# Optimization experiments

Hardware: AMD Instinct MI355X
Metric: run time of the kernel (lower is better)

Reference implementation:

```python
import jax, jax.numpy as jnp
import numpy as np

BS, GRID, LSTM_H, CNN_C, PROJ = 256, 49, 512, 2048, 512


def setup_inputs() -> dict:
    key = jax.random.key(0)
    ks = jax.random.split(key, 7)
    s = lambda fan_in: 1.0 / np.sqrt(fan_in)
    return {
        "lstm_hidden": jax.random.normal(ks[0], (BS, LSTM_H), jnp.float32),
        "cnn_feat": jax.random.normal(ks[1], (BS, GRID, CNN_C), jnp.float32),
        "W_lstm": jax.random.normal(ks[2], (PROJ, LSTM_H), jnp.float32) * s(LSTM_H),
        "b_lstm": jax.random.normal(ks[3], (PROJ,), jnp.float32) * s(LSTM_H),
        "W_cnn": jax.random.normal(ks[4], (PROJ, CNN_C), jnp.float32) * s(CNN_C),
        "b_cnn": jax.random.normal(ks[5], (PROJ,), jnp.float32) * s(CNN_C),
        "w_attn": jax.random.normal(ks[6], (1, PROJ), jnp.float32) * s(PROJ),
    }


def reference(lstm_hidden, cnn_feat, W_lstm, b_lstm, W_cnn, b_cnn, w_attn):
    # H computed once (original loop recomputes it per grid, identically)
    H = lstm_hidden @ W_lstm.T + b_lstm                       # (bs, P)
    V = jnp.einsum("bgc,pc->bgp", cnn_feat, W_cnn) + b_cnn    # (bs, G, P)
    z = jnp.tanh(H[:, None, :] + V) @ w_attn[0]               # (bs, G)
    bs, G = z.shape
    # Faithful to torch: cat over grids along dim 0 -> (G*bs,), then view(bs, G)
    z_scrambled = jnp.swapaxes(z, 0, 1).reshape(bs, G)
    return jax.nn.softmax(z_scrambled, axis=1)
```

## Files before the change

kernel.cpp:

```cpp
#include <hip/hip_runtime.h>
#include <math.h>

#define BSZ    256
#define GRID_N 49
#define LSTMH  512
#define CNN_C  2048
#define PROJ   512
#define KAUG   2560
#define M_TOT  12544
#define BK     64
#define KTILES (KAUG / BK)

#define MT     64
#define NT     128
#define NBLK   ((M_TOT / MT) * (PROJ / NT))

#define ACHUNKS (M_TOT * CNN_C / 8)
#define LCHUNKS (BSZ * LSTMH / 8)
#define ABLK    ((ACHUNKS + LCHUNKS) / 256)
#define WBLK    640
#define PBLK    (ABLK + WBLK)

typedef short bf16x8 __attribute__((ext_vector_type(8)));
typedef float f32x4  __attribute__((ext_vector_type(4)));

static __device__ __forceinline__ unsigned short bf16_rne(float f) {
    unsigned int u = __float_as_uint(f);
    u = u + 0x7FFFu + ((u >> 16) & 1u);
    return (unsigned short)(u >> 16);
}
static __device__ __forceinline__ uint4 pack8f(const float* f) {
    uint4 o;
    o.x = (unsigned int)bf16_rne(f[0]) | ((unsigned int)bf16_rne(f[1]) << 16);
    o.y = (unsigned int)bf16_rne(f[2]) | ((unsigned int)bf16_rne(f[3]) << 16);
    o.z = (unsigned int)bf16_rne(f[4]) | ((unsigned int)bf16_rne(f[5]) << 16);
    o.w = (unsigned int)bf16_rne(f[6]) | ((unsigned int)bf16_rne(f[7]) << 16);
    return o;
}
static __device__ __forceinline__ float tanh_fast(float x) {
    float e = __expf(2.f * x);
    return 1.f - 2.f / (e + 1.f);
}
static __device__ __forceinline__ void glds16(const void* g, void* l) {
    __builtin_amdgcn_global_load_lds(
        (const __attribute__((address_space(1))) unsigned int*)g,
        (__attribute__((address_space(3))) unsigned int*)l, 16, 0, 0);
}

__global__ __launch_bounds__(256) void prep_all(
    const float* __restrict__ cnn, const float* __restrict__ lstm,
    const float* __restrict__ Wc,  const float* __restrict__ Wl,
    unsigned short* __restrict__ wsW, unsigned short* __restrict__ wsA,
    unsigned short* __restrict__ wsL, float* __restrict__ out)
{
    const int bid = blockIdx.x, t = threadIdx.x;
    if (bid < 49) out[bid * 256 + t] = 0.f;
    float f[8];
    if (bid < ABLK) {
        const int c = bid * 256 + t;
        const float* src; unsigned short* dst;
        if (c < ACHUNKS) { src = cnn  + (size_t)c * 8; dst = wsA + (size_t)c * 8; }
        else { const int c2 = c - ACHUNKS; src = lstm + (size_t)c2 * 8; dst = wsL + (size_t)c2 * 8; }
        *(float4*)&f[0] = ((const float4*)src)[0];
        *(float4*)&f[4] = ((const float4*)src)[1];
        *(uint4*)dst = pack8f(f);
    } else {
        const int c  = (bid - ABLK) * 256 + t;
        const int p  = c / 320;
        const int kc = (c % 320) * 8;
        const float* src = (kc < CNN_C) ? (Wc + (size_t)p * CNN_C + kc)
                                        : (Wl + (size_t)p * LSTMH + (kc - CNN_C));
        *(float4*)&f[0] = ((const float4*)src)[0];
        *(float4*)&f[4] = ((const float4*)src)[1];
        *(uint4*)(wsW + (size_t)p * KAUG + kc) = pack8f(f);
    }
}

__global__ __launch_bounds__(256, 4) void gemm6(
    const unsigned short* __restrict__ wsW, const unsigned short* __restrict__ wsA,
    const unsigned short* __restrict__ wsL,
    const float* __restrict__ bl, const float* __restrict__ bc,
    const float* __restrict__ wat, float* __restrict__ out)
{
    __shared__ unsigned short Ash[MT][BK];
    __shared__ unsigned short Bsh[NT][BK];

    const int t   = threadIdx.x;
    const int w   = t >> 6;
    const int l   = t & 63;
    const int q   = l >> 4;
    const int r16 = l & 15;

    const int bid = (int)blockIdx.x;
    const int swz = (bid & 7) * (NBLK / 8) + (bid >> 3);
    const int m0  = (swz >> 2) * MT;
    const int n0  = (swz & 3) * NT;

    const int srow = l >> 3;
    const int cg   = (l & 7) ^ srow;

    auto stage = [&](int kt) {
        const int k0 = kt * BK;
        #pragma unroll
        for (int j = 0; j < 4; ++j) {
            const int rowb = w * 32 + j * 8;
            const unsigned short* g = wsW + (size_t)(n0 + rowb + srow) * KAUG + k0 + cg * 8;
            glds16(g, &Bsh[rowb][0]);
        }
        if (k0 < CNN_C) {
            #pragma unroll
            for (int j = 0; j < 2; ++j) {
                const int rowa = w * 16 + j * 8;
                const unsigned short* g = wsA + (size_t)(m0 + rowa + srow) * CNN_C + k0 + cg * 8;
                glds16(g, &Ash[rowa][0]);
            }
        } else {
            const int k0l = k0 - CNN_C;
            #pragma unroll
            for (int j = 0; j < 2; ++j) {
                const int rowa = w * 16 + j * 8;
                const int rg   = m0 + rowa + srow;
                const unsigned short* g = wsL + (size_t)(rg / 49) * LSTMH + k0l + cg * 8;
                glds16(g, &Ash[rowa][0]);
            }
        }
    };

    f32x4 acc[4][2];
    #pragma unroll
    for (int mt = 0; mt < 4; ++mt)
        #pragma unroll
        for (int nt = 0; nt < 2; ++nt)
            acc[mt][nt] = (f32x4){0.f, 0.f, 0.f, 0.f};

    stage(0);

    for (int kt = 0; kt < KTILES; ++kt) {
        asm volatile("s_waitcnt vmcnt(0)" ::: "memory");
        __builtin_amdgcn_s_barrier();
        #pragma unroll
        for (int ks = 0; ks < 2; ++ks) {
            const int cp = ((ks * 4 + q) ^ (r16 & 7)) * 8;
            bf16x8 af[4], bfr[2];
            #pragma unroll
            for (int mt = 0; mt < 4; ++mt)
                af[mt] = *(const bf16x8*)&Ash[mt * 16 + r16][cp];
            #pragma unroll
            for (int nt = 0; nt < 2; ++nt)
                bfr[nt] = *(const bf16x8*)&Bsh[w * 32 + nt * 16 + r16][cp];
            #pragma unroll
            for (int mt = 0; mt < 4; ++mt)
                #pragma unroll
                for (int nt = 0; nt < 2; ++nt)
                    acc[mt][nt] = __builtin_amdgcn_mfma_f32_16x16x32_bf16(
                        af[mt], bfr[nt], acc[mt][nt], 0, 0, 0);
        }
        __builtin_amdgcn_s_barrier();
        if (kt + 1 < KTILES) stage(kt + 1);
    }

    float* zpf = (float*)&Ash[0][0];
    float part[4][4];
    #pragma unroll
    for (int mt = 0; mt < 4; ++mt)
        #pragma unroll
        for (int rr = 0; rr < 4; ++rr) part[mt][rr] = 0.f;
    #pragma unroll
    for (int nt = 0; nt < 2; ++nt) {
        const int p = n0 + w * 32 + nt * 16 + r16;
        const float bb = bl[p] + bc[p];
        const float wa = wat[p];
        #pragma unroll
        for (int mt = 0; mt < 4; ++mt)
            #pragma unroll
            for (int rr = 0; rr < 4; ++rr)
                part[mt][rr] += tanh_fast(acc[mt][nt][rr] + bb) * wa;
    }
    #pragma unroll
    for (int mt = 0; mt < 4; ++mt)
        #pragma unroll
        for (int rr = 0; rr < 4; ++rr) {
            float v = part[mt][rr];
            v += __shfl_xor(v, 1);
            v += __shfl_xor(v, 2);
            v += __shfl_xor(v, 4);
            v += __shfl_xor(v, 8);
            if (r16 == 0) zpf[w * MT + mt * 16 + q * 4 + rr] = v;
        }
    __syncthreads();
    if (t < MT) {
        const float v = zpf[t] + zpf[MT + t] + zpf[2 * MT + t] + zpf[3 * MT + t];
        const int row = m0 + t;
        const int b2  = row / 49;
        const int g2  = row - b2 * 49;
        atomicAdd(&out[g2 * BSZ + b2], v);
    }
}

__global__ __launch_bounds__(256, 4) void gemm_k(
    const float* __restrict__ lstm, const float* __restrict__ cnn,
    const float* __restrict__ Wc,   const float* __restrict__ Wl,
    const float* __restrict__ bl,   const float* __restrict__ bc,
    const float* __restrict__ wat,  float* __restrict__ out)
{
    __shared__ unsigned short Ash[MT][BK];
    __shared__ unsigned short Bsh[NT][BK];
    __shared__ float zp[4][MT];

    const int t   = threadIdx.x;
    const int w   = t >> 6;
    const int l   = t & 63;
    const int q   = l >> 4;
    const int r16 = l & 15;

    const int bid = (int)blockIdx.x;
    const int swz = (bid & 7) * (NBLK / 8) + (bid >> 3);
    const int m0 = (swz >> 2) * MT;
    const int n0 = (swz & 3) * NT;

    const int ra  = t >> 2;
    const int ca0 = t & 3;
    const int sa  = ra & 7;
    const int grow = m0 + ra;
    const int ab   = grow / 49;
    const int ag   = grow - ab * 49;
    const float* cnnb  = cnn + ((size_t)ab * GRID_N + ag) * CNN_C;
    const float* lstmb = lstm + (size_t)ab * LSTMH;

    f32x4 acc[4][2];
    #pragma unroll
    for (int mt = 0; mt < 4; ++mt)
        #pragma unroll
        for (int nt = 0; nt < 2; ++nt)
            acc[mt][nt] = (f32x4){0.f, 0.f, 0.f, 0.f};

    float4 fa0, fa1, fa2, fa3;

    auto a_load = [&](int k0) {
        const float* s = (k0 < CNN_C) ? (cnnb + k0) : (lstmb + (k0 - CNN_C));
        const float4* p0 = (const float4*)(s + ca0 * 8);
        const float4* p1 = (const float4*)(s + (ca0 + 4) * 8);
        fa0 = p0[0]; fa1 = p0[1];
        fa2 = p1[0]; fa3 = p1[1];
    };
    auto a_write = [&]() {
        float f[8];
        *(float4*)&f[0] = fa0; *(float4*)&f[4] = fa1;
        *(uint4*)&Ash[ra][(ca0 ^ sa) * 8] = pack8f(f);
        *(float4*)&f[0] = fa2; *(float4*)&f[4] = fa3;
        *(uint4*)&Ash[ra][((ca0 + 4) ^ sa) * 8] = pack8f(f);
    };
    auto b_stage = [&](int k0) {
        const int rb = t >> 1;
        const int hb = t & 1;
        const float* s = (k0 < CNN_C) ? (Wc + (size_t)(n0 + rb) * CNN_C + k0)
                                      : (Wl + (size_t)(n0 + rb) * LSTMH + (k0 - CNN_C));
        const int sw = rb & 7;
        #pragma unroll
        for (int c = 0; c < 4; ++c) {
            const int cc = hb * 4 + c;
            float f[8];
            *(float4*)&f[0] = ((const float4*)(s + cc * 8))[0];
            *(float4*)&f[4] = ((const float4*)(s + cc * 8))[1];
            *(uint4*)&Bsh[rb][(cc ^ sw) * 8] = pack8f(f);
        }
    };

    a_load(0);
    a_write();
    b_stage(0);

    for (int kt = 0; kt < KTILES; ++kt) {
        __syncthreads();
        const bool more = (kt + 1 < KTILES);
        if (more) a_load((kt + 1) * BK);
        #pragma unroll
        for (int ks = 0; ks < 2; ++ks) {
            const int cp = ((ks * 4 + q) ^ (r16 & 7)) * 8;
            bf16x8 af[4], bfr[2];
            #pragma unroll
            for (int mt = 0; mt < 4; ++mt)
                af[mt] = *(const bf16x8*)&Ash[mt * 16 + r16][cp];
            #pragma unroll
            for (int nt = 0; nt < 2; ++nt)
                bfr[nt] = *(const bf16x8*)&Bsh[w * 32 + nt * 16 + r16][cp];
            #pragma unroll
            for (int mt = 0; mt < 4; ++mt)
                #pragma unroll
                for (int nt = 0; nt < 2; ++nt)
                    acc[mt][nt] = __builtin_amdgcn_mfma_f32_16x16x32_bf16(
                        af[mt], bfr[nt], acc[mt][nt], 0, 0, 0);
        }
        __syncthreads();
        if (more) { a_write(); b_stage((kt + 1) * BK); }
    }

    float part[4][4];
    #pragma unroll
    for (int mt = 0; mt < 4; ++mt)
        #pragma unroll
        for (int rr = 0; rr < 4; ++rr) part[mt][rr] = 0.f;
    #pragma unroll
    for (int nt = 0; nt < 2; ++nt) {
        const int p = n0 + w * 32 + nt * 16 + r16;
        const float bb = bl[p] + bc[p];
        const float wa = wat[p];
        #pragma unroll
        for (int mt = 0; mt < 4; ++mt)
            #pragma unroll
            for (int rr = 0; rr < 4; ++rr)
                part[mt][rr] += tanh_fast(acc[mt][nt][rr] + bb) * wa;
    }
    #pragma unroll
    for (int mt = 0; mt < 4; ++mt)
        #pragma unroll
        for (int rr = 0; rr < 4; ++rr) {
            float v = part[mt][rr];
            v += __shfl_xor(v, 1);
            v += __shfl_xor(v, 2);
            v += __shfl_xor(v, 4);
            v += __shfl_xor(v, 8);
            if (r16 == 0) zp[w][mt * 16 + q * 4 + rr] = v;
        }
    __syncthreads();
    if (t < MT) {
        const float v = zp[0][t] + zp[1][t] + zp[2][t] + zp[3][t];
        const int row = m0 + t;
        const int b2  = row / 49;
        const int g2  = row - b2 * 49;
        atomicAdd(&out[g2 * BSZ + b2], v);
    }
}

__global__ __launch_bounds__(64) void softmax_rows(float* __restrict__ out)
{
    const int i = blockIdx.x;
    const int j = threadIdx.x;
    float x = (j < GRID_N) ? out[i * GRID_N + j] : -1e30f;
    float m = x;
    #pragma unroll
    for (int off = 32; off > 0; off >>= 1) m = fmaxf(m, __shfl_xor(m, off));
    float e = (j < GRID_N) ? __expf(x - m) : 0.f;
    float s = e;
    #pragma unroll
    for (int off = 32; off > 0; off >>= 1) s += __shfl_xor(s, off);
    if (j < GRID_N) out[i * GRID_N + j] = e / s;
}

extern "C" void kernel_launch(void* const* d_in, const int* in_sizes, int n_in,
                              void* d_out, int out_size, void* d_ws, size_t ws_size,
                              hipStream_t stream)
{
    const float* lstm = (const float*)d_in[0];
    const float* cnn  = (const float*)d_in[1];
    const float* Wl   = (const float*)d_in[2];
    const float* bl   = (const float*)d_in[3];
    const float* Wc   = (const float*)d_in[4];
    const float* bc   = (const float*)d_in[5];
    const float* wat  = (const float*)d_in[6];
    float* out = (float*)d_out;

    const size_t szW = (size_t)PROJ * KAUG * sizeof(unsigned short);
    const size_t szA = (size_t)M_TOT * CNN_C * sizeof(unsigned short);
    const size_t szL = (size_t)BSZ * LSTMH * sizeof(unsigned short);

    if (ws_size >= szW + szA + szL) {
        unsigned short* wsW = (unsigned short*)d_ws;
        unsigned short* wsA = wsW + (size_t)PROJ * KAUG;
        unsigned short* wsL = wsA + (size_t)M_TOT * CNN_C;
        prep_all<<<dim3(PBLK), dim3(256), 0, stream>>>(cnn, lstm, Wc, Wl, wsW, wsA, wsL, out);
        gemm6<<<dim3(NBLK), dim3(256), 0, stream>>>(wsW, wsA, wsL, bl, bc, wat, out);
    } else {
        hipMemsetAsync(out, 0, (size_t)out_size * sizeof(float), stream);
        gemm_k<<<dim3(NBLK), dim3(256), 0, stream>>>(lstm, cnn, Wc, Wl, bl, bc, wat, out);
    }
    softmax_rows<<<dim3(BSZ), dim3(64), 0, stream>>>(out);
}
```

Baseline: 219.1 us.

## Double-buffer GEMM LDS tiles and use grid-stride loop in prep kernel

The GEMM now keeps two LDS buffers for A and B and issues the global-to-LDS loads for the next K tile before computing on the current one, so memory latency overlaps with MFMA work and only one barrier is needed per iteration. The prep kernel switches from one chunk per thread to a grid-stride loop over a fixed 1792-block grid that covers activations, LSTM and weights together. Double buffering doubles LDS use per block (to 48KB), which may cut occupancy below the four blocks per CU requested by the launch bounds.

Result: slower. 245.6 us (+12.1%).

```diff
diff --git a/kernel.cpp b/kernel.cpp
--- a/kernel.cpp
+++ b/kernel.cpp
@@ -17,9 +17,10 @@
 
 #define ACHUNKS (M_TOT * CNN_C / 8)
 #define LCHUNKS (BSZ * LSTMH / 8)
-#define ABLK    ((ACHUNKS + LCHUNKS) / 256)
-#define WBLK    640
-#define PBLK    (ABLK + WBLK)
+#define WCHUNKS (PROJ * KAUG / 8)
+#define TOTCHUNK (ACHUNKS + LCHUNKS + WCHUNKS)
+#define PGRID   1792
+#define PSTEP   (PGRID * 256)
 
 typedef short bf16x8 __attribute__((ext_vector_type(8)));
 typedef float f32x4  __attribute__((ext_vector_type(4)));
@@ -47,7 +48,7 @@
         (__attribute__((address_space(3))) unsigned int*)l, 16, 0, 0);
 }
 
-__global__ __launch_bounds__(256) void prep_all(
+__global__ __launch_bounds__(256) void prep_all2(
     const float* __restrict__ cnn, const float* __restrict__ lstm,
     const float* __restrict__ Wc,  const float* __restrict__ Wl,
     unsigned short* __restrict__ wsW, unsigned short* __restrict__ wsA,
@@ -55,35 +56,36 @@
 {
     const int bid = blockIdx.x, t = threadIdx.x;
     if (bid < 49) out[bid * 256 + t] = 0.f;
-    float f[8];
-    if (bid < ABLK) {
-        const int c = bid * 256 + t;
+    for (int c = bid * 256 + t; c < TOTCHUNK; c += PSTEP) {
         const float* src; unsigned short* dst;
-        if (c < ACHUNKS) { src = cnn  + (size_t)c * 8; dst = wsA + (size_t)c * 8; }
-        else { const int c2 = c - ACHUNKS; src = lstm + (size_t)c2 * 8; dst = wsL + (size_t)c2 * 8; }
+        if (c < ACHUNKS) {
+            src = cnn + (size_t)c * 8; dst = wsA + (size_t)c * 8;
+        } else if (c < ACHUNKS + LCHUNKS) {
+            const int c2 = c - ACHUNKS;
+            src = lstm + (size_t)c2 * 8; dst = wsL + (size_t)c2 * 8;
+        } else {
+            const int c3 = c - ACHUNKS - LCHUNKS;
+            const int p  = c3 / 320;
+            const int kc = (c3 % 320) * 8;
+            src = (kc < CNN_C) ? (Wc + (size_t)p * CNN_C + kc)
+                               : (Wl + (size_t)p * LSTMH + (kc - CNN_C));
+            dst = wsW + (size_t)p * KAUG + kc;
+        }
+        float f[8];
         *(float4*)&f[0] = ((const float4*)src)[0];
         *(float4*)&f[4] = ((const float4*)src)[1];
         *(uint4*)dst = pack8f(f);
-    } else {
-        const int c  = (bid - ABLK) * 256 + t;
-        const int p  = c / 320;
-        const int kc = (c % 320) * 8;
-        const float* src = (kc < CNN_C) ? (Wc + (size_t)p * CNN_C + kc)
-                                        : (Wl + (size_t)p * LSTMH + (kc - CNN_C));
-        *(float4*)&f[0] = ((const float4*)src)[0];
-        *(float4*)&f[4] = ((const float4*)src)[1];
-        *(uint4*)(wsW + (size_t)p * KAUG + kc) = pack8f(f);
-    }
-}
-
-__global__ __launch_bounds__(256, 4) void gemm6(
+    }
+}
+
+__global__ __launch_bounds__(256, 4) void gemm7(
     const unsigned short* __restrict__ wsW, const unsigned short* __restrict__ wsA,
     const unsigned short* __restrict__ wsL,
     const float* __restrict__ bl, const float* __restrict__ bc,
     const float* __restrict__ wat, float* __restrict__ out)
 {
-    __shared__ unsigned short Ash[MT][BK];
-    __shared__ unsigned short Bsh[NT][BK];
+    __shared__ unsigned short Ab[2][MT][BK];
+    __shared__ unsigned short Bb[2][NT][BK];
 
     const int t   = threadIdx.x;
     const int w   = t >> 6;
@@ -99,20 +101,20 @@
     const int srow = l >> 3;
     const int cg   = (l & 7) ^ srow;
 
-    auto stage = [&](int kt) {
+    auto stage = [&](int kt, int bufi) {
         const int k0 = kt * BK;
         #pragma unroll
         for (int j = 0; j < 4; ++j) {
             const int rowb = w * 32 + j * 8;
             const unsigned short* g = wsW + (size_t)(n0 + rowb + srow) * KAUG + k0 + cg * 8;
-            glds16(g, &Bsh[rowb][0]);
+            glds16(g, &Bb[bufi][rowb][0]);
         }
         if (k0 < CNN_C) {
             #pragma unroll
             for (int j = 0; j < 2; ++j) {
                 const int rowa = w * 16 + j * 8;
                 const unsigned short* g = wsA + (size_t)(m0 + rowa + srow) * CNN_C + k0 + cg * 8;
-                glds16(g, &Ash[rowa][0]);
+                glds16(g, &Ab[bufi][rowa][0]);
             }
         } else {
             const int k0l = k0 - CNN_C;
@@ -121,7 +123,7 @@
                 const int rowa = w * 16 + j * 8;
                 const int rg   = m0 + rowa + srow;
                 const unsigned short* g = wsL + (size_t)(rg / 49) * LSTMH + k0l + cg * 8;
-                glds16(g, &Ash[rowa][0]);
+                glds16(g, &Ab[bufi][rowa][0]);
             }
         }
     };
@@ -133,21 +135,23 @@
         for (int nt = 0; nt < 2; ++nt)
             acc[mt][nt] = (f32x4){0.f, 0.f, 0.f, 0.f};
 
-    stage(0);
-
+    stage(0, 0);
+    asm volatile("s_waitcnt vmcnt(0)" ::: "memory");
+    __builtin_amdgcn_s_barrier();
+
+    int cur = 0;
     for (int kt = 0; kt < KTILES; ++kt) {
-        asm volatile("s_waitcnt vmcnt(0)" ::: "memory");
-        __builtin_amdgcn_s_barrier();
+        if (kt + 1 < KTILES) stage(kt + 1, cur ^ 1);
         #pragma unroll
         for (int ks = 0; ks < 2; ++ks) {
             const int cp = ((ks * 4 + q) ^ (r16 & 7)) * 8;
             bf16x8 af[4], bfr[2];
             #pragma unroll
             for (int mt = 0; mt < 4; ++mt)
-                af[mt] = *(const bf16x8*)&Ash[mt * 16 + r16][cp];
+                af[mt] = *(const bf16x8*)&Ab[cur][mt * 16 + r16][cp];
             #pragma unroll
             for (int nt = 0; nt < 2; ++nt)
-                bfr[nt] = *(const bf16x8*)&Bsh[w * 32 + nt * 16 + r16][cp];
+                bfr[nt] = *(const bf16x8*)&Bb[cur][w * 32 + nt * 16 + r16][cp];
             #pragma unroll
             for (int mt = 0; mt < 4; ++mt)
                 #pragma unroll
@@ -155,11 +159,12 @@
                     acc[mt][nt] = __builtin_amdgcn_mfma_f32_16x16x32_bf16(
                         af[mt], bfr[nt], acc[mt][nt], 0, 0, 0);
         }
+        asm volatile("s_waitcnt vmcnt(0) lgkmcnt(0)" ::: "memory");
         __builtin_amdgcn_s_barrier();
-        if (kt + 1 < KTILES) stage(kt + 1);
-    }
-
-    float* zpf = (float*)&Ash[0][0];
+        cur ^= 1;
+    }
+
+    float* zpf = (float*)&Ab[0][0][0];
     float part[4][4];
     #pragma unroll
     for (int mt = 0; mt < 4; ++mt)
@@ -368,8 +373,8 @@
         unsigned short* wsW = (unsigned short*)d_ws;
         unsigned short* wsA = wsW + (size_t)PROJ * KAUG;
         unsigned short* wsL = wsA + (size_t)M_TOT * CNN_C;
-        prep_all<<<dim3(PBLK), dim3(256), 0, stream>>>(cnn, lstm, Wc, Wl, wsW, wsA, wsL, out);
-        gemm6<<<dim3(NBLK), dim3(256), 0, stream>>>(wsW, wsA, wsL, bl, bc, wat, out);
+        prep_all2<<<dim3(PGRID), dim3(256), 0, stream>>>(cnn, lstm, Wc, Wl, wsW, wsA, wsL, out);
+        gemm7<<<dim3(NBLK), dim3(256), 0, stream>>>(wsW, wsA, wsL, bl, bc, wat, out);
     } else {
         hipMemsetAsync(out, 0, (size_t)out_size * sizeof(float), stream);
         gemm_k<<<dim3(NBLK), dim3(256), 0, stream>>>(lstm, cnn, Wc, Wl, bl, bc, wat, out);
```
